# Kernel optimization log

Measured on AMD Instinct MI355X. Metric: run time of the kernel, lower is better.

The kernel has to match this reference:

```python
import jax, jax.numpy as jnp
import numpy as np

NUM_WORDS = 200000
EMBED = 128
B = 16384
WIN = 8
N_LABELS = 10
PR_W = 0.5
S1 = 1.0
S2 = 0.2


def setup_inputs() -> dict:
    key = jax.random.key(0)
    ks = jax.random.split(key, 13)
    u = lambda k, s: jax.random.uniform(k, s, jnp.float32, -1.0, 1.0)
    return {
        'inputs': jax.random.randint(ks[0], (B, 1), 0, NUM_WORDS),
        'outputs': jax.random.randint(ks[1], (B, WIN), 0, NUM_WORDS),
        'covars': jax.random.randint(ks[2], (B, 1), 0, N_LABELS),
        'noise': jax.random.randint(ks[3], (B, WIN), 0, NUM_WORDS),
        'wt': jnp.ones((1,), jnp.float32),
        'eps_in': jax.random.normal(ks[4], (B, 1, EMBED), jnp.float32),
        'eps_out': jax.random.normal(ks[5], (B, WIN, EMBED), jnp.float32),
        'in_w': u(ks[6], (NUM_WORDS, EMBED)),
        'out_w': u(ks[7], (NUM_WORDS, EMBED)),
        'in_rho_w': u(ks[8], (NUM_WORDS, EMBED)),
        'out_rho_w': u(ks[9], (NUM_WORDS, EMBED)),
        'cov_w': u(ks[10], (N_LABELS, EMBED)),
        'lin_w': jax.random.normal(ks[11], (EMBED, 2 * EMBED), jnp.float32) * 0.05,
        'lin_b': jax.random.normal(ks[12], (EMBED,), jnp.float32) * 0.05,
    }


def _prior(w):
    # log( pw*N-ish(s1) + (1-pw)*N-ish(s2) ), summed over embed dim
    n1 = PR_W * jnp.exp(-w ** 2 / (2.0 * S1 ** 2))
    n2 = (1.0 - PR_W) * jnp.exp(-w ** 2 / (2.0 * S2 ** 2))
    return jnp.sum(jnp.log(n1 + n2), axis=1)


def _forward(inputs, outputs, covars, noise, wt, eps_in, eps_out,
             in_w, out_w, in_rho_w, out_rho_w, cov_w, lin_w, lin_b):
    b, win = outputs.shape
    e = in_w.shape[1]
    flat = lambda v: jnp.broadcast_to(v, (b, win, e)).reshape(-1, e)

    y = cov_w[jnp.broadcast_to(covars, (b, win)).reshape(-1)]      # [bw, e]

    mu_in = flat(in_w[inputs])                                     # [bw, e]
    eps_in_f = flat(eps_in)
    sig_in = flat(jax.nn.softplus(in_rho_w[inputs]))               # log(exp(rho)+1)
    w_in = jnp.tanh(jnp.concatenate([mu_in, y], axis=1) @ lin_w.T + lin_b) + sig_in * eps_in_f
    post_in = -0.5 * jnp.sum(eps_in_f ** 2, axis=1) - jnp.sum(jnp.log(sig_in), axis=1)
    prior_in = _prior(w_in)

    mu_out = flat(out_w[outputs])
    eps_out_f = flat(eps_out)
    sig_out = flat(jax.nn.softplus(out_rho_w[outputs]))
    w_out = mu_out + sig_out * eps_out_f
    post_out = -0.5 * jnp.sum(eps_out_f ** 2, axis=1) - jnp.sum(jnp.log(sig_out), axis=1)
    prior_out = _prior(w_out)

    log_target = jnp.log(jax.nn.sigmoid(jnp.sum(w_in * w_out, axis=1)))
    noise_e = -out_w[noise].reshape(-1, e)
    log_sampled = jnp.log(jax.nn.sigmoid(jnp.sum(w_in * noise_e, axis=1)))

    likelihood = log_target + log_sampled
    loss = wt[0] * (post_in + post_out - prior_in - prior_out) - likelihood
    return jnp.mean(loss)


def reference(inputs, outputs, covars, noise, wt, eps_in, eps_out,
              in_w, out_w, in_rho_w, out_rho_w, cov_w, lin_w, lin_b):
    return _forward(inputs, outputs, covars, noise, wt, eps_in, eps_out,
                    in_w, out_w, in_rho_w, out_rho_w, cov_w, lin_w, lin_b)
```

## Files before the change

### kernel.cpp

```cpp
#include <hip/hip_runtime.h>
#include <hip/hip_bf16.h>

#define NUM_WORDS 200000
#define EMBED 128
#define BATCH 16384
#define WIN 8
#define B_PER_BLK 8
#define GRID (BATCH / B_PER_BLK)

typedef __attribute__((ext_vector_type(8))) short short8;
typedef __attribute__((ext_vector_type(4))) float f32x4;

#define LN_HALF (-0.69314718056f)

__device__ __forceinline__ short f2bf(float f) {
  unsigned u = __float_as_uint(f);
  u = u + 0x7FFFu + ((u >> 16) & 1u);
  return (short)(u >> 16);
}

__device__ __forceinline__ float sp(float x) {
  return fmaxf(x, 0.f) + __logf(1.f + __expf(-fabsf(x)));
}

__global__ void prep_kernel(const float* __restrict__ lin_w,
                            const float* __restrict__ lin_b,
                            const float* __restrict__ cov_w,
                            short* __restrict__ bpack,
                            float* __restrict__ covp) {
  int t = blockIdx.x * 256 + threadIdx.x;
  if (t < 16384) {
    int e  = t & 7;
    int l  = (t >> 3) & 63;
    int jt = (t >> 9) & 1;
    int kk = (t >> 10) & 3;
    int wv = (t >> 12) & 3;
    int j = wv * 32 + jt * 16 + (l & 15);
    int k = kk * 32 + (l >> 4) * 8 + e;
    bpack[t] = f2bf(lin_w[j * 256 + k]);
  } else if (t < 16384 + 1280) {
    int u = t - 16384;
    int c = u >> 7, j = u & 127;
    float s = lin_b[j];
    for (int k = 0; k < 128; ++k)
      s += cov_w[c * 128 + k] * lin_w[j * 256 + 128 + k];
    covp[u] = s;
  }
}

__global__ __launch_bounds__(256, 5) void main_kernel(
    const int* __restrict__ inputs, const int* __restrict__ outputs,
    const int* __restrict__ covars, const int* __restrict__ noise,
    const float* __restrict__ wtp,
    const float* __restrict__ eps_in, const float* __restrict__ eps_out,
    const float* __restrict__ in_w, const float* __restrict__ out_w,
    const float* __restrict__ in_rho_w, const float* __restrict__ out_rho_w,
    const short* __restrict__ bpack, const float* __restrict__ covp,
    double* __restrict__ parts) {
  __shared__ float w_s[B_PER_BLK][132];
  __shared__ float red_s[4];

  const int tid  = threadIdx.x;
  const int lane = tid & 63;
  const int wv   = tid >> 6;
  const int q    = lane >> 4;
  const int f16  = lane & 15;
  const int bbase = blockIdx.x * B_PER_BLK;
  const float wtv = wtp[0];

  short8 bfrag[4][2];
  const int4* bp = (const int4*)bpack;
  #pragma unroll
  for (int kk = 0; kk < 4; ++kk) {
    #pragma unroll
    for (int jt = 0; jt < 2; ++jt) {
      int fi = (wv * 4 + kk) * 2 + jt;
      int4 v = bp[fi * 64 + lane];
      bfrag[kk][jt] = __builtin_bit_cast(short8, v);
    }
  }

  int idxA = inputs[bbase + (f16 & (B_PER_BLK - 1))];
  f32x4 acc0 = {0.f, 0.f, 0.f, 0.f}, acc1 = {0.f, 0.f, 0.f, 0.f};
  #pragma unroll
  for (int kk = 0; kk < 4; ++kk) {
    const float* ap = in_w + (size_t)idxA * 128 + kk * 32 + q * 8;
    float4 a0 = *(const float4*)ap;
    float4 a1 = *(const float4*)(ap + 4);
    short8 af;
    af[0] = f2bf(a0.x); af[1] = f2bf(a0.y); af[2] = f2bf(a0.z); af[3] = f2bf(a0.w);
    af[4] = f2bf(a1.x); af[5] = f2bf(a1.y); af[6] = f2bf(a1.z); af[7] = f2bf(a1.w);
    acc0 = __builtin_amdgcn_mfma_f32_16x16x32_bf16(af, bfrag[kk][0], acc0, 0, 0, 0);
    acc1 = __builtin_amdgcn_mfma_f32_16x16x32_bf16(af, bfrag[kk][1], acc1, 0, 0, 0);
  }
  #pragma unroll
  for (int r = 0; r < 4; ++r) {
    int row = q * 4 + r;
    if (row < B_PER_BLK) {
      w_s[row][wv * 32 + f16]      = acc0[r];
      w_s[row][wv * 32 + 16 + f16] = acc1[r];
    }
  }
  __syncthreads();

  float accum = 0.f;

  {
    const int b  = tid >> 5;
    const int j  = (tid & 31) * 4;
    const int gb = bbase + b;
    const int idx = inputs[gb];
    const int cov = covars[gb];

    float4 wp = *(const float4*)(&w_s[b][j]);
    float4 rh = *(const float4*)(in_rho_w + (size_t)idx * 128 + j);
    float4 ep = *(const float4*)(eps_in + (size_t)gb * 128 + j);
    float4 cv = *(const float4*)(covp + cov * 128 + j);

    float rha[4] = {rh.x, rh.y, rh.z, rh.w};
    float epa[4] = {ep.x, ep.y, ep.z, ep.w};
    float xa[4]  = {wp.x + cv.x, wp.y + cv.y, wp.z + cv.z, wp.w + cv.w};

    float wi4[4];
    float se2 = 0.f, sw2 = 0.f, ps = 1.f, pu = 1.f;
    #pragma unroll
    for (int e = 0; e < 4; ++e) {
      float es = __expf(rha[e]);
      float s  = __logf(1.f + es);
      float x  = fminf(fmaxf(xa[e], -15.f), 15.f);
      float e2 = __expf(2.f * x);
      float th = (e2 - 1.f) / (e2 + 1.f);
      float w  = th + s * epa[e];
      wi4[e] = w;
      float u  = __expf(-12.f * w * w);
      ps *= s; pu *= (1.f + u);
      se2 += epa[e] * epa[e];
      sw2 += w * w;
    }
    *(float4*)(&w_s[b][j]) = make_float4(wi4[0], wi4[1], wi4[2], wi4[3]);
    float t1 = -0.5f * se2 - __logf(ps) + 0.5f * sw2 - 4.f * LN_HALF - __logf(pu);
    accum = 8.f * wtv * t1;
  }
  __syncthreads();

  {
    const int g  = tid >> 3;
    const int f8 = tid & 7;

    const int rlA = g,       rlB = 32 + g;
    const int bA  = rlA >> 3, bB  = rlB >> 3;
    const int rA  = (bbase + bA) * 8 + (rlA & 7);
    const int rB  = (bbase + bB) * 8 + (rlB & 7);
    const int oA  = outputs[rA], nzA = noise[rA];
    const int oB  = outputs[rB], nzB = noise[rB];

    #pragma unroll
    for (int it = 0; it < 2; ++it) {
      const int o  = it ? oB : oA;
      const int nz = it ? nzB : nzA;
      const int r  = it ? rB : rA;
      const int b2 = it ? bB : bA;
      const float* wrow = out_w     + (size_t)o  * 128;
      const float* rrow = out_rho_w + (size_t)o  * 128;
      const float* erow = eps_out   + (size_t)r  * 128;
      const float* nrow = out_w     + (size_t)nz * 128;

      float4 mo[4], ro[4], eo[4], nv[4];
      #pragma unroll
      for (int c = 0; c < 4; ++c) {
        const int off = (c * 8 + f8) * 4;
        mo[c] = *(const float4*)(wrow + off);
        ro[c] = *(const float4*)(rrow + off);
        eo[c] = *(const float4*)(erow + off);
        nv[c] = *(const float4*)(nrow + off);
      }

      float d1 = 0.f, d2 = 0.f, se2 = 0.f, sw2 = 0.f;
      float ps = 1.f, pu = 1.f;

      #pragma unroll
      for (int c = 0; c < 4; ++c) {
        const int off = (c * 8 + f8) * 4;
        float4 wi = *(const float4*)(&w_s[b2][off]);
        float moa[4] = {mo[c].x, mo[c].y, mo[c].z, mo[c].w};
        float roa[4] = {ro[c].x, ro[c].y, ro[c].z, ro[c].w};
        float eoa[4] = {eo[c].x, eo[c].y, eo[c].z, eo[c].w};
        float nva[4] = {nv[c].x, nv[c].y, nv[c].z, nv[c].w};
        float wia[4] = {wi.x, wi.y, wi.z, wi.w};

        #pragma unroll
        for (int e = 0; e < 4; ++e) {
          float es = __expf(roa[e]);
          float s  = __logf(1.f + es);
          float wo = fmaf(s, eoa[e], moa[e]);
          float u  = __expf(-12.f * wo * wo);
          ps *= s;
          pu *= (1.f + u);
          se2 += eoa[e] * eoa[e];
          sw2 += wo * wo;
          d1  += wia[e] * wo;
          d2  += wia[e] * nva[e];
        }
      }
      float t2 = -0.5f * se2 - __logf(ps) + 0.5f * sw2 - 16.f * LN_HALF - __logf(pu);
      accum += wtv * t2;

      d1 += __shfl_xor(d1, 1, 64); d1 += __shfl_xor(d1, 2, 64); d1 += __shfl_xor(d1, 4, 64);
      d2 += __shfl_xor(d2, 1, 64); d2 += __shfl_xor(d2, 2, 64); d2 += __shfl_xor(d2, 4, 64);
      if (f8 == 0) accum += sp(-d1) + sp(d2);
    }
  }

  #pragma unroll
  for (int m = 1; m <= 32; m <<= 1) accum += __shfl_xor(accum, m, 64);
  if (lane == 0) red_s[wv] = accum;
  __syncthreads();
  if (tid == 0) {
    double s = (double)red_s[0] + (double)red_s[1] + (double)red_s[2] + (double)red_s[3];
    parts[blockIdx.x] = s;
  }
}

__global__ void fin_kernel(const double* __restrict__ parts, float* __restrict__ out) {
  __shared__ double s[256];
  const int tid = threadIdx.x;
  double a = 0.0;
  for (int i = tid; i < GRID; i += 256) a += parts[i];
  s[tid] = a;
  __syncthreads();
  for (int st = 128; st > 0; st >>= 1) {
    if (tid < st) s[tid] += s[tid + st];
    __syncthreads();
  }
  if (tid == 0) out[0] = (float)(s[0] / (double)(BATCH * WIN));
}

extern "C" void kernel_launch(void* const* d_in, const int* in_sizes, int n_in,
                              void* d_out, int out_size, void* d_ws, size_t ws_size,
                              hipStream_t stream) {
  const int*   inputs    = (const int*)d_in[0];
  const int*   outputs   = (const int*)d_in[1];
  const int*   covars    = (const int*)d_in[2];
  const int*   noise     = (const int*)d_in[3];
  const float* wt        = (const float*)d_in[4];
  const float* eps_in    = (const float*)d_in[5];
  const float* eps_out   = (const float*)d_in[6];
  const float* in_w      = (const float*)d_in[7];
  const float* out_w     = (const float*)d_in[8];
  const float* in_rho_w  = (const float*)d_in[9];
  const float* out_rho_w = (const float*)d_in[10];
  const float* cov_w     = (const float*)d_in[11];
  const float* lin_w     = (const float*)d_in[12];
  const float* lin_b     = (const float*)d_in[13];

  short*  bpack = (short*)d_ws;
  float*  covp  = (float*)((char*)d_ws + 32768);
  double* parts = (double*)((char*)d_ws + 40960);

  prep_kernel<<<69, 256, 0, stream>>>(lin_w, lin_b, cov_w, bpack, covp);
  main_kernel<<<GRID, 256, 0, stream>>>(inputs, outputs, covars, noise, wt,
                                        eps_in, eps_out, in_w, out_w,
                                        in_rho_w, out_rho_w, bpack, covp, parts);
  fin_kernel<<<1, 256, 0, stream>>>(parts, (float*)d_out);
}
```

Measured before the change: 64.23 us.

## Fuse prep kernel into main kernel and drop inter-phase block barrier

Removes the separate prep kernel that pre-packed lin_w into bf16 fragments and precomputed the covariate projection. Each block now loads lin_w from fp32, converts it on the fly, and runs the covariate half of the linear layer as four extra MFMA steps. The work is remapped so each wave touches only its own batch rows, which lets the second __syncthreads become a compiler memory fence. This saves one kernel launch and a barrier, but adds redundant per-block lin_w loads and conversions and lowers the occupancy hint from 5 to 4.

```diff
diff --git a/kernel.cpp b/kernel.cpp
--- a/kernel.cpp
+++ b/kernel.cpp
@@ -19,43 +19,26 @@
   return (short)(u >> 16);
 }
 
+__device__ __forceinline__ short8 pack8(float4 a0, float4 a1) {
+  short8 r;
+  r[0] = f2bf(a0.x); r[1] = f2bf(a0.y); r[2] = f2bf(a0.z); r[3] = f2bf(a0.w);
+  r[4] = f2bf(a1.x); r[5] = f2bf(a1.y); r[6] = f2bf(a1.z); r[7] = f2bf(a1.w);
+  return r;
+}
+
 __device__ __forceinline__ float sp(float x) {
   return fmaxf(x, 0.f) + __logf(1.f + __expf(-fabsf(x)));
 }
 
-__global__ void prep_kernel(const float* __restrict__ lin_w,
-                            const float* __restrict__ lin_b,
-                            const float* __restrict__ cov_w,
-                            short* __restrict__ bpack,
-                            float* __restrict__ covp) {
-  int t = blockIdx.x * 256 + threadIdx.x;
-  if (t < 16384) {
-    int e  = t & 7;
-    int l  = (t >> 3) & 63;
-    int jt = (t >> 9) & 1;
-    int kk = (t >> 10) & 3;
-    int wv = (t >> 12) & 3;
-    int j = wv * 32 + jt * 16 + (l & 15);
-    int k = kk * 32 + (l >> 4) * 8 + e;
-    bpack[t] = f2bf(lin_w[j * 256 + k]);
-  } else if (t < 16384 + 1280) {
-    int u = t - 16384;
-    int c = u >> 7, j = u & 127;
-    float s = lin_b[j];
-    for (int k = 0; k < 128; ++k)
-      s += cov_w[c * 128 + k] * lin_w[j * 256 + 128 + k];
-    covp[u] = s;
-  }
-}
-
-__global__ __launch_bounds__(256, 5) void main_kernel(
+__global__ __launch_bounds__(256, 4) void main_kernel(
     const int* __restrict__ inputs, const int* __restrict__ outputs,
     const int* __restrict__ covars, const int* __restrict__ noise,
     const float* __restrict__ wtp,
     const float* __restrict__ eps_in, const float* __restrict__ eps_out,
     const float* __restrict__ in_w, const float* __restrict__ out_w,
     const float* __restrict__ in_rho_w, const float* __restrict__ out_rho_w,
-    const short* __restrict__ bpack, const float* __restrict__ covp,
+    const float* __restrict__ cov_w, const float* __restrict__ lin_w,
+    const float* __restrict__ lin_b,
     double* __restrict__ parts) {
   __shared__ float w_s[B_PER_BLK][132];
   __shared__ float red_s[4];
@@ -68,37 +51,42 @@
   const int bbase = blockIdx.x * B_PER_BLK;
   const float wtv = wtp[0];
 
-  short8 bfrag[4][2];
-  const int4* bp = (const int4*)bpack;
-  #pragma unroll
-  for (int kk = 0; kk < 4; ++kk) {
-    #pragma unroll
-    for (int jt = 0; jt < 2; ++jt) {
-      int fi = (wv * 4 + kk) * 2 + jt;
-      int4 v = bp[fi * 64 + lane];
-      bfrag[kk][jt] = __builtin_bit_cast(short8, v);
-    }
-  }
-
-  int idxA = inputs[bbase + (f16 & (B_PER_BLK - 1))];
-  f32x4 acc0 = {0.f, 0.f, 0.f, 0.f}, acc1 = {0.f, 0.f, 0.f, 0.f};
-  #pragma unroll
-  for (int kk = 0; kk < 4; ++kk) {
-    const float* ap = in_w + (size_t)idxA * 128 + kk * 32 + q * 8;
-    float4 a0 = *(const float4*)ap;
-    float4 a1 = *(const float4*)(ap + 4);
-    short8 af;
-    af[0] = f2bf(a0.x); af[1] = f2bf(a0.y); af[2] = f2bf(a0.z); af[3] = f2bf(a0.w);
-    af[4] = f2bf(a1.x); af[5] = f2bf(a1.y); af[6] = f2bf(a1.z); af[7] = f2bf(a1.w);
-    acc0 = __builtin_amdgcn_mfma_f32_16x16x32_bf16(af, bfrag[kk][0], acc0, 0, 0, 0);
-    acc1 = __builtin_amdgcn_mfma_f32_16x16x32_bf16(af, bfrag[kk][1], acc1, 0, 0, 0);
-  }
-  #pragma unroll
-  for (int r = 0; r < 4; ++r) {
-    int row = q * 4 + r;
-    if (row < B_PER_BLK) {
-      w_s[row][wv * 32 + f16]      = acc0[r];
-      w_s[row][wv * 32 + 16 + f16] = acc1[r];
+  const int g  = tid >> 3;
+  const int f8 = tid & 7;
+  const int rA = bbase * 8 + g;
+  const int rB = rA + 32;
+  const int oA = outputs[rA], nzA = noise[rA];
+  const int oB = outputs[rB], nzB = noise[rB];
+
+  {
+    const int bsel = f16 & (B_PER_BLK - 1);
+    const int idxA = inputs[bbase + bsel];
+    const int covA = covars[bbase + bsel];
+    const float* ar0 = in_w  + (size_t)idxA * 128 + q * 8;
+    const float* ar1 = cov_w + covA * 128 + q * 8;
+    const float* bptr = lin_w + (size_t)(wv * 32 + f16) * 256 + q * 8;
+
+    f32x4 acc0 = {0.f, 0.f, 0.f, 0.f}, acc1 = {0.f, 0.f, 0.f, 0.f};
+    #pragma unroll
+    for (int kk = 0; kk < 8; ++kk) {
+      const float* ap = (kk < 4) ? (ar0 + kk * 32) : (ar1 + (kk - 4) * 32);
+      float4 a0  = *(const float4*)ap;
+      float4 a1  = *(const float4*)(ap + 4);
+      float4 b00 = *(const float4*)(bptr + kk * 32);
+      float4 b01 = *(const float4*)(bptr + kk * 32 + 4);
+      float4 b10 = *(const float4*)(bptr + 16 * 256 + kk * 32);
+      float4 b11 = *(const float4*)(bptr + 16 * 256 + kk * 32 + 4);
+      short8 af = pack8(a0, a1);
+      acc0 = __builtin_amdgcn_mfma_f32_16x16x32_bf16(af, pack8(b00, b01), acc0, 0, 0, 0);
+      acc1 = __builtin_amdgcn_mfma_f32_16x16x32_bf16(af, pack8(b10, b11), acc1, 0, 0, 0);
+    }
+    #pragma unroll
+    for (int r = 0; r < 4; ++r) {
+      int row = q * 4 + r;
+      if (row < B_PER_BLK) {
+        w_s[row][wv * 32 + f16]      = acc0[r];
+        w_s[row][wv * 32 + 16 + f16] = acc1[r];
+      }
     }
   }
   __syncthreads();
@@ -106,20 +94,20 @@
   float accum = 0.f;
 
   {
-    const int b  = tid >> 5;
-    const int j  = (tid & 31) * 4;
+    const int h  = lane >> 5;
+    const int b  = wv + 4 * h;
+    const int jj = (lane & 31) * 4;
     const int gb = bbase + b;
     const int idx = inputs[gb];
-    const int cov = covars[gb];
-
-    float4 wp = *(const float4*)(&w_s[b][j]);
-    float4 rh = *(const float4*)(in_rho_w + (size_t)idx * 128 + j);
-    float4 ep = *(const float4*)(eps_in + (size_t)gb * 128 + j);
-    float4 cv = *(const float4*)(covp + cov * 128 + j);
+
+    float4 wp = *(const float4*)(&w_s[b][jj]);
+    float4 rh = *(const float4*)(in_rho_w + (size_t)idx * 128 + jj);
+    float4 ep = *(const float4*)(eps_in + (size_t)gb * 128 + jj);
+    float4 lb = *(const float4*)(lin_b + jj);
 
     float rha[4] = {rh.x, rh.y, rh.z, rh.w};
     float epa[4] = {ep.x, ep.y, ep.z, ep.w};
-    float xa[4]  = {wp.x + cv.x, wp.y + cv.y, wp.z + cv.z, wp.w + cv.w};
+    float xa[4]  = {wp.x + lb.x, wp.y + lb.y, wp.z + lb.z, wp.w + lb.w};
 
     float wi4[4];
     float se2 = 0.f, sw2 = 0.f, ps = 1.f, pu = 1.f;
@@ -137,29 +125,19 @@
       se2 += epa[e] * epa[e];
       sw2 += w * w;
     }
-    *(float4*)(&w_s[b][j]) = make_float4(wi4[0], wi4[1], wi4[2], wi4[3]);
+    *(float4*)(&w_s[b][jj]) = make_float4(wi4[0], wi4[1], wi4[2], wi4[3]);
     float t1 = -0.5f * se2 - __logf(ps) + 0.5f * sw2 - 4.f * LN_HALF - __logf(pu);
     accum = 8.f * wtv * t1;
   }
-  __syncthreads();
+  asm volatile("" ::: "memory");
 
   {
-    const int g  = tid >> 3;
-    const int f8 = tid & 7;
-
-    const int rlA = g,       rlB = 32 + g;
-    const int bA  = rlA >> 3, bB  = rlB >> 3;
-    const int rA  = (bbase + bA) * 8 + (rlA & 7);
-    const int rB  = (bbase + bB) * 8 + (rlB & 7);
-    const int oA  = outputs[rA], nzA = noise[rA];
-    const int oB  = outputs[rB], nzB = noise[rB];
-
     #pragma unroll
     for (int it = 0; it < 2; ++it) {
       const int o  = it ? oB : oA;
       const int nz = it ? nzB : nzA;
       const int r  = it ? rB : rA;
-      const int b2 = it ? bB : bA;
+      const int b2 = it ? (wv + 4) : wv;
       const float* wrow = out_w     + (size_t)o  * 128;
       const float* rrow = out_rho_w + (size_t)o  * 128;
       const float* erow = eps_out   + (size_t)r  * 128;
@@ -253,13 +231,11 @@
   const float* lin_w     = (const float*)d_in[12];
   const float* lin_b     = (const float*)d_in[13];
 
-  short*  bpack = (short*)d_ws;
-  float*  covp  = (float*)((char*)d_ws + 32768);
-  double* parts = (double*)((char*)d_ws + 40960);
-
-  prep_kernel<<<69, 256, 0, stream>>>(lin_w, lin_b, cov_w, bpack, covp);
+  double* parts = (double*)d_ws;
+
   main_kernel<<<GRID, 256, 0, stream>>>(inputs, outputs, covars, noise, wt,
                                         eps_in, eps_out, in_w, out_w,
-                                        in_rho_w, out_rho_w, bpack, covp, parts);
+                                        in_rho_w, out_rho_w, cov_w, lin_w,
+                                        lin_b, parts);
   fin_kernel<<<1, 256, 0, stream>>>(parts, (float*)d_out);
 }
```

Result: slower. 72.04 us (+12.2%).

## Fuse final reduction into main kernel via last-block atomic counter

Applied to the files above, without the earlier changes.

Removes the separate single-block finalize kernel: each block publishes its partial with a release store and bumps a global counter, and the last block to arrive reduces all partials and writes the mean. The counter is reset in the prep kernel. Launch bounds are also raised from 5 to 8 waves per SIMD to push occupancy. This saves one kernel launch and its dependency gap, but adds an atomic per block, extra shared memory for the fused reduction, and possible register spills under the tighter launch bound.

```diff
diff --git a/kernel.cpp b/kernel.cpp
--- a/kernel.cpp
+++ b/kernel.cpp
@@ -27,8 +27,10 @@
                             const float* __restrict__ lin_b,
                             const float* __restrict__ cov_w,
                             short* __restrict__ bpack,
-                            float* __restrict__ covp) {
+                            float* __restrict__ covp,
+                            unsigned* __restrict__ cnt) {
   int t = blockIdx.x * 256 + threadIdx.x;
+  if (t == 0) *cnt = 0u;
   if (t < 16384) {
     int e  = t & 7;
     int l  = (t >> 3) & 63;
@@ -48,7 +50,7 @@
   }
 }
 
-__global__ __launch_bounds__(256, 5) void main_kernel(
+__global__ __launch_bounds__(256, 8) void main_kernel(
     const int* __restrict__ inputs, const int* __restrict__ outputs,
     const int* __restrict__ covars, const int* __restrict__ noise,
     const float* __restrict__ wtp,
@@ -56,9 +58,12 @@
     const float* __restrict__ in_w, const float* __restrict__ out_w,
     const float* __restrict__ in_rho_w, const float* __restrict__ out_rho_w,
     const short* __restrict__ bpack, const float* __restrict__ covp,
-    double* __restrict__ parts) {
+    double* __restrict__ parts, unsigned* __restrict__ cnt,
+    float* __restrict__ out) {
   __shared__ float w_s[B_PER_BLK][132];
   __shared__ float red_s[4];
+  __shared__ int   last_s;
+  __shared__ double fs[256];
 
   const int tid  = threadIdx.x;
   const int lane = tid & 63;
@@ -217,22 +222,27 @@
   __syncthreads();
   if (tid == 0) {
     double s = (double)red_s[0] + (double)red_s[1] + (double)red_s[2] + (double)red_s[3];
-    parts[blockIdx.x] = s;
-  }
-}
-
-__global__ void fin_kernel(const double* __restrict__ parts, float* __restrict__ out) {
-  __shared__ double s[256];
-  const int tid = threadIdx.x;
-  double a = 0.0;
-  for (int i = tid; i < GRID; i += 256) a += parts[i];
-  s[tid] = a;
-  __syncthreads();
-  for (int st = 128; st > 0; st >>= 1) {
-    if (tid < st) s[tid] += s[tid + st];
+    __hip_atomic_store(&parts[blockIdx.x], s, __ATOMIC_RELEASE,
+                       __HIP_MEMORY_SCOPE_AGENT);
+    unsigned prev = __hip_atomic_fetch_add(cnt, 1u, __ATOMIC_ACQ_REL,
+                                           __HIP_MEMORY_SCOPE_AGENT);
+    last_s = (prev == GRID - 1) ? 1 : 0;
+  }
+  __syncthreads();
+
+  if (last_s) {
+    double a = 0.0;
+    for (int i = tid; i < GRID; i += 256)
+      a += __hip_atomic_load(&parts[i], __ATOMIC_ACQUIRE,
+                             __HIP_MEMORY_SCOPE_AGENT);
+    fs[tid] = a;
     __syncthreads();
-  }
-  if (tid == 0) out[0] = (float)(s[0] / (double)(BATCH * WIN));
+    for (int st = 128; st > 0; st >>= 1) {
+      if (tid < st) fs[tid] += fs[tid + st];
+      __syncthreads();
+    }
+    if (tid == 0) out[0] = (float)(fs[0] / (double)(BATCH * WIN));
+  }
 }
 
 extern "C" void kernel_launch(void* const* d_in, const int* in_sizes, int n_in,
@@ -253,13 +263,14 @@
   const float* lin_w     = (const float*)d_in[12];
   const float* lin_b     = (const float*)d_in[13];
 
-  short*  bpack = (short*)d_ws;
-  float*  covp  = (float*)((char*)d_ws + 32768);
-  double* parts = (double*)((char*)d_ws + 40960);
-
-  prep_kernel<<<69, 256, 0, stream>>>(lin_w, lin_b, cov_w, bpack, covp);
+  short*    bpack = (short*)d_ws;
+  float*    covp  = (float*)((char*)d_ws + 32768);
+  double*   parts = (double*)((char*)d_ws + 40960);
+  unsigned* cnt   = (unsigned*)((char*)d_ws + 57344);
+
+  prep_kernel<<<69, 256, 0, stream>>>(lin_w, lin_b, cov_w, bpack, covp, cnt);
   main_kernel<<<GRID, 256, 0, stream>>>(inputs, outputs, covars, noise, wt,
                                         eps_in, eps_out, in_w, out_w,
-                                        in_rho_w, out_rho_w, bpack, covp, parts);
-  fin_kernel<<<1, 256, 0, stream>>>(parts, (float*)d_out);
-}
+                                        in_rho_w, out_rho_w, bpack, covp,
+                                        parts, cnt, (float*)d_out);
+}
```

Result: slower. 192.4 us (+199.5%).
